# Performance work log

Hardware: AMD Instinct MI355X
Metric: run time of the kernel (lower is better)

The kernel has to match this reference:

```python
import jax, jax.numpy as jnp
import numpy as np

D_EMB = 1024
N_HEADS = 16


def setup_inputs() -> dict:
    key = jax.random.key(0)
    k_x, k_wq, k_bq, k_wp, k_bp = jax.random.split(key, 5)
    B, N, D = 8, 1024, D_EMB
    x = jax.random.normal(k_x, (B, N, D), dtype=jnp.float32)
    s = 1.0 / np.sqrt(D)
    w_qkv = jax.random.normal(k_wq, (D, 3 * D), dtype=jnp.float32) * s
    b_qkv = jax.random.normal(k_bq, (3 * D,), dtype=jnp.float32) * 0.01
    w_proj = jax.random.normal(k_wp, (D, D), dtype=jnp.float32) * s
    b_proj = jax.random.normal(k_bp, (D,), dtype=jnp.float32) * 0.01
    return {"x": x, "w_qkv": w_qkv, "b_qkv": b_qkv, "w_proj": w_proj, "b_proj": b_proj}


def reference(x, w_qkv, b_qkv, w_proj, b_proj):
    B, N, D = x.shape
    H = N_HEADS
    d = D // H
    qkv = x @ w_qkv + b_qkv                      # [B, N, 3D]
    # einops '(h d qkv)': qkv index is the innermost factor of the last dim
    qkv = qkv.reshape(B, N, H, d, 3)
    q = qkv[..., 0]                              # [B, N, H, d]
    k = qkv[..., 1]
    v = qkv[..., 2]
    score = jnp.einsum('bqhd,bkhd->bhqk', q, k)  # [B, H, N, N]
    # module scales AFTER softmax, by sqrt(d_emb) (not sqrt(d_head))
    att = jax.nn.softmax(score, axis=-1) / jnp.sqrt(jnp.float32(D))
    out = jnp.einsum('bhqk,bkhd->bqhd', att, v).reshape(B, N, D)
    return out @ w_proj + b_proj
```

## Files before the change

### kernel.cpp

```cpp
#include <hip/hip_runtime.h>
#include <hip/hip_bf16.h>
#include <stdint.h>

typedef __hip_bfloat16 bf16;
typedef __attribute__((ext_vector_type(8))) short short8;
typedef __attribute__((ext_vector_type(4))) float f32x4;
typedef __attribute__((ext_vector_type(16))) float f32x16;

#define MFMA16(a, b, c) __builtin_amdgcn_mfma_f32_16x16x32_bf16(a, b, c, 0, 0, 0)
#define MFMA32(a, b, c) __builtin_amdgcn_mfma_f32_32x32x16_bf16(a, b, c, 0, 0, 0)

#define BATCH 8
#define SEQ   1024
#define DEMB  1024
#define NH    16
#define DH    64
#define MTOT  (BATCH * SEQ)

__device__ __forceinline__ float rdf(const void* p, size_t idx, int isf) {
  if (isf) return ((const float*)p)[idx];
  return __bfloat162float(((const bf16*)p)[idx]);
}

__device__ __forceinline__ unsigned int pk2(float a, float b) {
  unsigned short ua = __bfloat16_as_ushort(__float2bfloat16(a));
  unsigned short ub = __bfloat16_as_ushort(__float2bfloat16(b));
  return (unsigned int)ua | ((unsigned int)ub << 16);
}

union U4S8 { uint4 u; short8 s; };

__device__ __forceinline__ void gload16(const bf16* g, bf16* l) {
  __builtin_amdgcn_global_load_lds(
      (const __attribute__((address_space(1))) void*)g,
      (__attribute__((address_space(3))) void*)l, 16, 0, 0);
}

__global__ void detect_dtype(const unsigned int* __restrict__ xw, int* __restrict__ flag) {
  int lane = threadIdx.x;
  float v = __uint_as_float(xw[lane]);
  bool isf32 = (fabsf(v) < 1e20f);
  unsigned long long m = __ballot(isf32);
  if (lane == 0) flag[0] = (__popcll(m) >= 32) ? 1 : 0;
}

__global__ __launch_bounds__(256) void convert_x(
    const void* __restrict__ xin, bf16* __restrict__ xc, const int* __restrict__ flag) {
  const int isf = flag[0];
  size_t i = ((size_t)blockIdx.x * 256 + threadIdx.x) * 8;
  if (isf) {
    const float* xf = (const float*)xin;
    float4 a = *(const float4*)&xf[i];
    float4 b = *(const float4*)&xf[i + 4];
    bf16 o[8];
    o[0] = __float2bfloat16(a.x); o[1] = __float2bfloat16(a.y);
    o[2] = __float2bfloat16(a.z); o[3] = __float2bfloat16(a.w);
    o[4] = __float2bfloat16(b.x); o[5] = __float2bfloat16(b.y);
    o[6] = __float2bfloat16(b.z); o[7] = __float2bfloat16(b.w);
    *(int4*)&xc[i] = *(const int4*)&o[0];
  } else {
    *(int4*)&xc[i] = *(const int4*)&((const bf16*)xin)[i];
  }
}

__global__ __launch_bounds__(256) void permute_wqkv(
    const void* __restrict__ w, const void* __restrict__ b,
    bf16* __restrict__ wt, float* __restrict__ bqp, const int* __restrict__ flag) {
  __shared__ __attribute__((aligned(16))) bf16 ls[192][66];
  const int isf = flag[0];
  const int t = threadIdx.x;
  const int k0 = blockIdx.x * 64;
  const int h = blockIdx.y;
#pragma unroll
  for (int i = 0; i < 48; ++i) {
    int e = t + i * 256;
    int k = e / 192, c = e % 192;
    ls[c][k] = __float2bfloat16(rdf(w, (size_t)(k0 + k) * 3072 + h * 192 + c, isf));
  }
  if (blockIdx.x == 0 && t < 192) {
    int dd = t / 3, j = t % 3;
    bqp[j * 1024 + h * 64 + dd] = rdf(b, h * 192 + t, isf);
  }
  __syncthreads();
#pragma unroll
  for (int i = 0; i < 48; ++i) {
    int e = t + i * 256;
    int c = e / 64, k = e & 63;
    int dd = c / 3, j = c % 3;
    wt[(size_t)(j * 1024 + h * 64 + dd) * 1024 + k0 + k] = ls[c][k];
  }
}

__global__ __launch_bounds__(256) void transpose_wp(
    const void* __restrict__ w, bf16* __restrict__ wt, const int* __restrict__ flag) {
  __shared__ __attribute__((aligned(16))) bf16 ls[64][66];
  const int isf = flag[0];
  const int t = threadIdx.x;
  const int r0 = blockIdx.y * 64;
  const int c0 = blockIdx.x * 64;
#pragma unroll
  for (int i = 0; i < 16; ++i) {
    int e = t + i * 256;
    int r = e >> 6, c = e & 63;
    ls[c][r] = __float2bfloat16(rdf(w, (size_t)(r0 + r) * 1024 + c0 + c, isf));
  }
  __syncthreads();
#pragma unroll
  for (int i = 0; i < 16; ++i) {
    int e = t + i * 256;
    int c = e >> 6, r = e & 63;
    wt[(size_t)(c0 + c) * 1024 + r0 + r] = ls[c][r];
  }
}

__device__ __forceinline__ void gemm_core(
    const bf16* __restrict__ A, const bf16* __restrict__ Bt,
    int m0, int n0, f32x4 acc[4][4],
    bf16 lsA[128][32], bf16 lsB[128][32]) {
  const int t = threadIdx.x;
  const int lane = t & 63, w = t >> 6;
  const int quad = lane >> 4, col = lane & 15;
  const int wr = (w >> 1) * 64, wc = (w & 1) * 64;
  const int gr = lane >> 2;
  const int gc = (lane & 3) * 8;
  const bf16* gA = A + (size_t)(m0 + w * 32 + gr) * 1024 + gc;
  const bf16* gB = Bt + (size_t)(n0 + w * 32 + gr) * 1024 + gc;
  bf16* dA0 = &lsA[w * 32][0];
  bf16* dA1 = &lsA[w * 32 + 16][0];
  bf16* dB0 = &lsB[w * 32][0];
  bf16* dB1 = &lsB[w * 32 + 16][0];

  for (int kt = 0; kt < 1024; kt += 32) {
    __syncthreads();
    gload16(gA + kt, dA0);
    gload16(gA + 16 * 1024 + kt, dA1);
    gload16(gB + kt, dB0);
    gload16(gB + 16 * 1024 + kt, dB1);
    __syncthreads();
    short8 af[4], bfr[4];
#pragma unroll
    for (int i = 0; i < 4; ++i) af[i] = *(const short8*)&lsA[wr + i * 16 + col][quad * 8];
#pragma unroll
    for (int j = 0; j < 4; ++j) bfr[j] = *(const short8*)&lsB[wc + j * 16 + col][quad * 8];
#pragma unroll
    for (int i = 0; i < 4; ++i)
#pragma unroll
      for (int j = 0; j < 4; ++j)
        acc[i][j] = MFMA16(af[i], bfr[j], acc[i][j]);
  }
}

__global__ __launch_bounds__(256) void gemm_qkv(
    const bf16* __restrict__ A, const bf16* __restrict__ Bt,
    const float* __restrict__ bias,
    bf16* __restrict__ qb, bf16* __restrict__ kb, bf16* __restrict__ vb) {
  __shared__ __attribute__((aligned(16))) bf16 lsA[128][32];
  __shared__ __attribute__((aligned(16))) bf16 lsB[128][32];
  const int t = threadIdx.x;
  const int lane = t & 63, w = t >> 6;
  const int quad = lane >> 4, col = lane & 15;
  const int wr = (w >> 1) * 64, wc = (w & 1) * 64;
  const int m0 = blockIdx.y * 128;
  const int n0 = blockIdx.x * 128;
  f32x4 acc[4][4];
  const f32x4 zero = {0.f, 0.f, 0.f, 0.f};
#pragma unroll
  for (int i = 0; i < 4; ++i)
#pragma unroll
    for (int j = 0; j < 4; ++j) acc[i][j] = zero;

  gemm_core(A, Bt, m0, n0, acc, lsA, lsB);

  const int jj = n0 >> 10;
#pragma unroll
  for (int i = 0; i < 4; ++i) {
    int rbase = m0 + wr + i * 16 + quad * 4;
#pragma unroll
    for (int j = 0; j < 4; ++j) {
      int c = n0 + wc + j * 16 + col;
      int cc = c & 1023;
      int h = cc >> 6, dd = cc & 63;
      float bv = bias[c];
#pragma unroll
      for (int r = 0; r < 4; ++r) {
        int m = rbase + r;
        int bb = m >> 10, n = m & 1023;
        bf16 val = __float2bfloat16(acc[i][j][r] + bv);
        size_t bhq = (size_t)(bb * NH + h);
        if (jj == 0)      qb[(bhq * 1024 + n) * 64 + dd] = val;
        else if (jj == 1) kb[(bhq * 1024 + n) * 64 + dd] = val;
        else              vb[(bhq * 64 + dd) * 1024 + n] = val;
      }
    }
  }
}

__global__ __launch_bounds__(256, 4) void attn(
    const bf16* __restrict__ qb, const bf16* __restrict__ kb,
    const bf16* __restrict__ vb, bf16* __restrict__ ob) {
  const int t = threadIdx.x, lane = t & 63, w = t >> 6;
  const int q5 = lane & 31, half = lane >> 5;
  const int bh = blockIdx.y;
  const int bat = bh >> 4, h = bh & 15;
  const int q0 = blockIdx.x * 128;
  const int qrow = q0 + w * 32 + q5;

  __shared__ __attribute__((aligned(16))) bf16 lsK[64][72];
  __shared__ __attribute__((aligned(16))) bf16 lsV[64][72];

  const bf16* qp = qb + (size_t)bh * (1024 * 64);
  const bf16* kp = kb + (size_t)bh * (1024 * 64);
  const bf16* vp = vb + (size_t)bh * (64 * 1024);

  short8 bq[4];
#pragma unroll
  for (int kk = 0; kk < 4; ++kk)
    bq[kk] = *(const short8*)&qp[(size_t)qrow * 64 + kk * 16 + half * 8];

  float m_run = -1e30f, l_run = 0.f;
  f32x16 po[2];
#pragma unroll
  for (int r = 0; r < 16; ++r) { po[0][r] = 0.f; po[1][r] = 0.f; }

  const int sr = t >> 3;
  const int sc = (t & 7) * 8;

  for (int kt = 0; kt < 1024; kt += 64) {
    int4 g0 = *(const int4*)&kp[(size_t)(kt + sr) * 64 + sc];
    int4 g1 = *(const int4*)&kp[(size_t)(kt + 32 + sr) * 64 + sc];
    int4 g2 = *(const int4*)&vp[(size_t)sr * 1024 + kt + sc];
    int4 g3 = *(const int4*)&vp[(size_t)(32 + sr) * 1024 + kt + sc];
    __syncthreads();
    *(int4*)&lsK[sr][sc] = g0;
    *(int4*)&lsK[32 + sr][sc] = g1;
    *(int4*)&lsV[sr][sc] = g2;
    *(int4*)&lsV[32 + sr][sc] = g3;
    __syncthreads();

    f32x16 st[2];
#pragma unroll
    for (int r = 0; r < 16; ++r) { st[0][r] = 0.f; st[1][r] = 0.f; }
#pragma unroll
    for (int kk = 0; kk < 4; ++kk) {
#pragma unroll
      for (int tj = 0; tj < 2; ++tj) {
        short8 ak = *(const short8*)&lsK[tj * 32 + q5][kk * 16 + half * 8];
        st[tj] = MFMA32(ak, bq[kk], st[tj]);
      }
    }

    float smax = st[0][0];
#pragma unroll
    for (int r = 1; r < 16; ++r) smax = fmaxf(smax, st[0][r]);
#pragma unroll
    for (int r = 0; r < 16; ++r) smax = fmaxf(smax, st[1][r]);
    smax = fmaxf(smax, __shfl_xor(smax, 32));
    float mnew = fmaxf(m_run, smax);
    float alpha = __expf(m_run - mnew);
    m_run = mnew;
    float lsum = 0.f;
#pragma unroll
    for (int tj = 0; tj < 2; ++tj)
#pragma unroll
      for (int r = 0; r < 16; ++r) {
        float p = __expf(st[tj][r] - mnew);
        st[tj][r] = p;
        lsum += p;
      }
    lsum += __shfl_xor(lsum, 32);
    l_run = l_run * alpha + lsum;
#pragma unroll
    for (int r = 0; r < 16; ++r) { po[0][r] *= alpha; po[1][r] *= alpha; }

#pragma unroll
    for (int kk2 = 0; kk2 < 4; ++kk2) {
      const int nbA = 2 * kk2, nbB = 2 * kk2 + 1;
      unsigned int a0 = pk2(st[nbA >> 2][4 * (nbA & 3) + 0], st[nbA >> 2][4 * (nbA & 3) + 1]);
      unsigned int a1 = pk2(st[nbA >> 2][4 * (nbA & 3) + 2], st[nbA >> 2][4 * (nbA & 3) + 3]);
      unsigned int b0 = pk2(st[nbB >> 2][4 * (nbB & 3) + 0], st[nbB >> 2][4 * (nbB & 3) + 1]);
      unsigned int b1 = pk2(st[nbB >> 2][4 * (nbB & 3) + 2], st[nbB >> 2][4 * (nbB & 3) + 3]);
      unsigned int s0 = half ? a0 : b0;
      unsigned int s1 = half ? a1 : b1;
      unsigned int r0 = (unsigned int)__shfl_xor((int)s0, 32);
      unsigned int r1 = (unsigned int)__shfl_xor((int)s1, 32);
      U4S8 fr;
      fr.u.x = half ? r0 : a0;
      fr.u.y = half ? r1 : a1;
      fr.u.z = half ? b0 : r0;
      fr.u.w = half ? b1 : r1;
#pragma unroll
      for (int ti = 0; ti < 2; ++ti) {
        short8 av = *(const short8*)&lsV[ti * 32 + q5][kk2 * 16 + half * 8];
        po[ti] = MFMA32(av, fr.s, po[ti]);
      }
    }
  }

  float inv = 1.0f / (l_run * 32.0f);
  bf16* op = ob + ((size_t)(bat * 1024 + qrow)) * 1024 + h * 64;
#pragma unroll
  for (int ti = 0; ti < 2; ++ti)
#pragma unroll
    for (int g = 0; g < 4; ++g) {
      unsigned int lo = pk2(po[ti][4 * g + 0] * inv, po[ti][4 * g + 1] * inv);
      unsigned int hi = pk2(po[ti][4 * g + 2] * inv, po[ti][4 * g + 3] * inv);
      uint2 u = make_uint2(lo, hi);
      *(uint2*)&op[ti * 32 + g * 8 + half * 4] = u;
    }
}

__global__ __launch_bounds__(256) void gemm_proj(
    const bf16* __restrict__ A, const bf16* __restrict__ Bt,
    const void* __restrict__ bias, float* __restrict__ out,
    const int* __restrict__ flag) {
  __shared__ __attribute__((aligned(16))) bf16 lsA[128][32];
  __shared__ __attribute__((aligned(16))) bf16 lsB[128][32];
  const int isf = flag[0];
  const int t = threadIdx.x;
  const int lane = t & 63, w = t >> 6;
  const int quad = lane >> 4, col = lane & 15;
  const int wr = (w >> 1) * 64, wc = (w & 1) * 64;
  const int m0 = blockIdx.y * 128;
  const int n0 = blockIdx.x * 128;
  f32x4 acc[4][4];
  const f32x4 zero = {0.f, 0.f, 0.f, 0.f};
#pragma unroll
  for (int i = 0; i < 4; ++i)
#pragma unroll
    for (int j = 0; j < 4; ++j) acc[i][j] = zero;

  gemm_core(A, Bt, m0, n0, acc, lsA, lsB);

#pragma unroll
  for (int i = 0; i < 4; ++i) {
    int rbase = m0 + wr + i * 16 + quad * 4;
#pragma unroll
    for (int j = 0; j < 4; ++j) {
      int c = n0 + wc + j * 16 + col;
      float bv = rdf(bias, c, isf);
#pragma unroll
      for (int r = 0; r < 4; ++r)
        out[(size_t)(rbase + r) * 1024 + c] = acc[i][j][r] + bv;
    }
  }
}

extern "C" void kernel_launch(void* const* d_in, const int* in_sizes, int n_in,
                              void* d_out, int out_size, void* d_ws, size_t ws_size,
                              hipStream_t stream) {
  const void* x      = d_in[0];
  const void* w_qkv  = d_in[1];
  const void* b_qkv  = d_in[2];
  const void* w_proj = d_in[3];
  const void* b_proj = d_in[4];
  float* out = (float*)d_out;

  char* ws = (char*)d_ws;
  bf16*  wt_qkv = (bf16*)(ws);
  float* bqp    = (float*)(ws + 6291456);
  bf16*  wtp    = (bf16*)(ws + 6303744);
  bf16*  xc     = (bf16*)(ws + 8400896);
  bf16*  q_buf  = (bf16*)(ws + 25178112);
  bf16*  k_buf  = (bf16*)(ws + 41955328);
  bf16*  v_buf  = (bf16*)(ws + 58732544);
  int*   flag   = (int*)(ws + 75509760);
  bf16*  att    = xc;

  detect_dtype<<<1, 64, 0, stream>>>((const unsigned int*)x, flag);
  convert_x<<<4096, 256, 0, stream>>>(x, xc, flag);
  permute_wqkv<<<dim3(16, 16), 256, 0, stream>>>(w_qkv, b_qkv, wt_qkv, bqp, flag);
  transpose_wp<<<dim3(16, 16), 256, 0, stream>>>(w_proj, wtp, flag);
  gemm_qkv<<<dim3(24, 64), 256, 0, stream>>>(xc, wt_qkv, bqp, q_buf, k_buf, v_buf);
  attn<<<dim3(8, 128), 256, 0, stream>>>(q_buf, k_buf, v_buf, att);
  gemm_proj<<<dim3(8, 64), 256, 0, stream>>>(att, wtp, b_proj, out, flag);
}
```

Baseline: 301.4 us.

## Replace GEMM core with 256x256 tiles and a 4-stage LDS pipeline

```diff
diff --git a/kernel.cpp b/kernel.cpp
--- a/kernel.cpp
+++ b/kernel.cpp
@@ -113,83 +113,126 @@
   }
 }
 
-__device__ __forceinline__ void gemm_core(
+__device__ __forceinline__ void gemm256_core(
     const bf16* __restrict__ A, const bf16* __restrict__ Bt,
-    int m0, int n0, f32x4 acc[4][4],
-    bf16 lsA[128][32], bf16 lsB[128][32]) {
+    int m0, int n0, bf16* lds, f32x4 acc[8][4]) {
   const int t = threadIdx.x;
   const int lane = t & 63, w = t >> 6;
-  const int quad = lane >> 4, col = lane & 15;
-  const int wr = (w >> 1) * 64, wc = (w & 1) * 64;
-  const int gr = lane >> 2;
-  const int gc = (lane & 3) * 8;
-  const bf16* gA = A + (size_t)(m0 + w * 32 + gr) * 1024 + gc;
-  const bf16* gB = Bt + (size_t)(n0 + w * 32 + gr) * 1024 + gc;
-  bf16* dA0 = &lsA[w * 32][0];
-  bf16* dA1 = &lsA[w * 32 + 16][0];
-  bf16* dB0 = &lsB[w * 32][0];
-  bf16* dB1 = &lsB[w * 32 + 16][0];
-
-  for (int kt = 0; kt < 1024; kt += 32) {
-    __syncthreads();
-    gload16(gA + kt, dA0);
-    gload16(gA + 16 * 1024 + kt, dA1);
-    gload16(gB + kt, dB0);
-    gload16(gB + 16 * 1024 + kt, dB1);
-    __syncthreads();
-    short8 af[4], bfr[4];
-#pragma unroll
-    for (int i = 0; i < 4; ++i) af[i] = *(const short8*)&lsA[wr + i * 16 + col][quad * 8];
-#pragma unroll
-    for (int j = 0; j < 4; ++j) bfr[j] = *(const short8*)&lsB[wc + j * 16 + col][quad * 8];
+  const int l15 = lane & 15, quad = lane >> 4;
+  const int wm = w >> 2, wn = w & 3;
+
+  const int sr = lane >> 2;
+  const int sc = (lane & 3) * 8;
+  const bf16* gA = A + (size_t)(m0 + w * 16 + sr) * 1024 + sc;
+  const bf16* gB = Bt + (size_t)(n0 + w * 16 + sr) * 1024 + sc;
+
+#pragma unroll
+  for (int tt = 0; tt < 3; ++tt) {
+    bf16* sb = lds + tt * 16384;
+    gload16(gA + tt * 32, sb + w * 512);
+    gload16(gA + tt * 32 + 131072, sb + 4096 + w * 512);
+    gload16(gB + tt * 32, sb + 8192 + w * 512);
+    gload16(gB + tt * 32 + 131072, sb + 12288 + w * 512);
+  }
+  asm volatile("s_waitcnt vmcnt(8)" ::: "memory");
+  __builtin_amdgcn_s_barrier();
+
+#pragma unroll 4
+  for (int tau = 0; tau < 32; ++tau) {
+    const int slot = tau & 3;
+    const int pf = (tau + 3) & 3;
+    const int kpf = ((tau + 3) & 31) * 32;
+    const bf16* ls = lds + slot * 16384;
+    bf16* sb = lds + pf * 16384;
+
+    short8 afr[4], bfr[4];
+    const bf16* pa0 = ls + (wm * 128 + l15) * 32 + quad * 8;
+#pragma unroll
+    for (int i = 0; i < 4; ++i) afr[i] = *(const short8*)(pa0 + i * 512);
+    const bf16* pb0 = ls + 8192 + (wn * 64 + l15) * 32 + quad * 8;
+#pragma unroll
+    for (int j = 0; j < 4; ++j) bfr[j] = *(const short8*)(pb0 + j * 512);
+    gload16(gA + kpf, sb + w * 512);
+    gload16(gA + kpf + 131072, sb + 4096 + w * 512);
+    asm volatile("" ::: "memory");
+    __builtin_amdgcn_s_barrier();
+    asm volatile("s_waitcnt lgkmcnt(0)" ::: "memory");
+    __builtin_amdgcn_s_setprio(1);
 #pragma unroll
     for (int i = 0; i < 4; ++i)
 #pragma unroll
       for (int j = 0; j < 4; ++j)
-        acc[i][j] = MFMA16(af[i], bfr[j], acc[i][j]);
-  }
-}
-
-__global__ __launch_bounds__(256) void gemm_qkv(
+        acc[i][j] = MFMA16(afr[i], bfr[j], acc[i][j]);
+    __builtin_amdgcn_s_setprio(0);
+    asm volatile("" ::: "memory");
+    __builtin_amdgcn_s_barrier();
+
+    const bf16* pa1 = pa0 + 64 * 32;
+#pragma unroll
+    for (int i = 0; i < 4; ++i) afr[i] = *(const short8*)(pa1 + i * 512);
+    gload16(gB + kpf, sb + 8192 + w * 512);
+    gload16(gB + kpf + 131072, sb + 12288 + w * 512);
+    asm volatile("" ::: "memory");
+    __builtin_amdgcn_s_barrier();
+    asm volatile("s_waitcnt lgkmcnt(0)" ::: "memory");
+    __builtin_amdgcn_s_setprio(1);
+#pragma unroll
+    for (int i = 0; i < 4; ++i)
+#pragma unroll
+      for (int j = 0; j < 4; ++j)
+        acc[4 + i][j] = MFMA16(afr[i], bfr[j], acc[4 + i][j]);
+    __builtin_amdgcn_s_setprio(0);
+    asm volatile("s_waitcnt vmcnt(8)" ::: "memory");
+    asm volatile("" ::: "memory");
+    __builtin_amdgcn_s_barrier();
+  }
+  asm volatile("s_waitcnt vmcnt(0)" ::: "memory");
+}
+
+__global__ __launch_bounds__(512, 2) void gemm256_qkv(
     const bf16* __restrict__ A, const bf16* __restrict__ Bt,
     const float* __restrict__ bias,
     bf16* __restrict__ qb, bf16* __restrict__ kb, bf16* __restrict__ vb) {
-  __shared__ __attribute__((aligned(16))) bf16 lsA[128][32];
-  __shared__ __attribute__((aligned(16))) bf16 lsB[128][32];
+  extern __shared__ bf16 smem[];
   const int t = threadIdx.x;
-  const int lane = t & 63, w = t >> 6;
-  const int quad = lane >> 4, col = lane & 15;
-  const int wr = (w >> 1) * 64, wc = (w & 1) * 64;
-  const int m0 = blockIdx.y * 128;
-  const int n0 = blockIdx.x * 128;
-  f32x4 acc[4][4];
+  const int lane = t & 63;
+  const int l15 = lane & 15, quad = lane >> 4;
+  const int w = t >> 6, wm = w >> 2, wn = w & 3;
+  const int bid = blockIdx.x;
+  const int swz = (bid & 7) * 48 + (bid >> 3);
+  const int m0 = (swz / 12) * 256;
+  const int n0 = (swz % 12) * 256;
+
+  f32x4 acc[8][4];
   const f32x4 zero = {0.f, 0.f, 0.f, 0.f};
 #pragma unroll
-  for (int i = 0; i < 4; ++i)
+  for (int i = 0; i < 8; ++i)
 #pragma unroll
     for (int j = 0; j < 4; ++j) acc[i][j] = zero;
 
-  gemm_core(A, Bt, m0, n0, acc, lsA, lsB);
+  gemm256_core(A, Bt, m0, n0, smem, acc);
 
   const int jj = n0 >> 10;
-#pragma unroll
-  for (int i = 0; i < 4; ++i) {
-    int rbase = m0 + wr + i * 16 + quad * 4;
-#pragma unroll
-    for (int j = 0; j < 4; ++j) {
-      int c = n0 + wc + j * 16 + col;
-      int cc = c & 1023;
-      int h = cc >> 6, dd = cc & 63;
-      float bv = bias[c];
-#pragma unroll
-      for (int r = 0; r < 4; ++r) {
-        int m = rbase + r;
-        int bb = m >> 10, n = m & 1023;
-        bf16 val = __float2bfloat16(acc[i][j][r] + bv);
-        size_t bhq = (size_t)(bb * NH + h);
-        if (jj == 0)      qb[(bhq * 1024 + n) * 64 + dd] = val;
-        else if (jj == 1) kb[(bhq * 1024 + n) * 64 + dd] = val;
-        else              vb[(bhq * 64 + dd) * 1024 + n] = val;
+  const int hh = ((n0 + wn * 64) & 1023) >> 6;
+#pragma unroll
+  for (int fi = 0; fi < 8; ++fi) {
+    int m = m0 + wm * 128 + fi * 16 + quad * 4;
+    int bb = m >> 10, nidx = m & 1023;
+    size_t bhq = (size_t)(bb * NH + hh);
+#pragma unroll
+    for (int fj = 0; fj < 4; ++fj) {
+      int dd = fj * 16 + l15;
+      float bv = bias[n0 + wn * 64 + dd];
+      if (jj == 2) {
+        unsigned int lo = pk2(acc[fi][fj][0] + bv, acc[fi][fj][1] + bv);
+        unsigned int hi = pk2(acc[fi][fj][2] + bv, acc[fi][fj][3] + bv);
+        *(uint2*)&vb[(bhq * 64 + dd) * 1024 + nidx] = make_uint2(lo, hi);
+      } else {
+        bf16* dst = (jj == 0) ? qb : kb;
+#pragma unroll
+        for (int r = 0; r < 4; ++r)
+          dst[(bhq * 1024 + (size_t)(nidx + r)) * 64 + dd] =
+              __float2bfloat16(acc[fi][fj][r] + bv);
       }
     }
   }
@@ -309,38 +352,40 @@
     }
 }
 
-__global__ __launch_bounds__(256) void gemm_proj(
+__global__ __launch_bounds__(512, 2) void gemm256_proj(
     const bf16* __restrict__ A, const bf16* __restrict__ Bt,
     const void* __restrict__ bias, float* __restrict__ out,
     const int* __restrict__ flag) {
-  __shared__ __attribute__((aligned(16))) bf16 lsA[128][32];
-  __shared__ __attribute__((aligned(16))) bf16 lsB[128][32];
+  extern __shared__ bf16 smem[];
+  const int t = threadIdx.x;
+  const int lane = t & 63;
+  const int l15 = lane & 15, quad = lane >> 4;
+  const int w = t >> 6, wm = w >> 2, wn = w & 3;
+  const int bid = blockIdx.x;
+  const int swz = (bid & 7) * 16 + (bid >> 3);
+  const int m0 = (swz >> 2) * 256;
+  const int n0 = (swz & 3) * 256;
+
+  f32x4 acc[8][4];
+  const f32x4 zero = {0.f, 0.f, 0.f, 0.f};
+#pragma unroll
+  for (int i = 0; i < 8; ++i)
+#pragma unroll
+    for (int j = 0; j < 4; ++j) acc[i][j] = zero;
+
+  gemm256_core(A, Bt, m0, n0, smem, acc);
+
   const int isf = flag[0];
-  const int t = threadIdx.x;
-  const int lane = t & 63, w = t >> 6;
-  const int quad = lane >> 4, col = lane & 15;
-  const int wr = (w >> 1) * 64, wc = (w & 1) * 64;
-  const int m0 = blockIdx.y * 128;
-  const int n0 = blockIdx.x * 128;
-  f32x4 acc[4][4];
-  const f32x4 zero = {0.f, 0.f, 0.f, 0.f};
-#pragma unroll
-  for (int i = 0; i < 4; ++i)
-#pragma unroll
-    for (int j = 0; j < 4; ++j) acc[i][j] = zero;
-
-  gemm_core(A, Bt, m0, n0, acc, lsA, lsB);
-
-#pragma unroll
-  for (int i = 0; i < 4; ++i) {
-    int rbase = m0 + wr + i * 16 + quad * 4;
-#pragma unroll
-    for (int j = 0; j < 4; ++j) {
-      int c = n0 + wc + j * 16 + col;
-      float bv = rdf(bias, c, isf);
+#pragma unroll
+  for (int fj = 0; fj < 4; ++fj) {
+    int c = n0 + wn * 64 + fj * 16 + l15;
+    float bv = rdf(bias, c, isf);
+#pragma unroll
+    for (int fi = 0; fi < 8; ++fi) {
+      int m = m0 + wm * 128 + fi * 16 + quad * 4;
 #pragma unroll
       for (int r = 0; r < 4; ++r)
-        out[(size_t)(rbase + r) * 1024 + c] = acc[i][j][r] + bv;
+        out[(size_t)(m + r) * 1024 + c] = acc[fi][fj][r] + bv;
     }
   }
 }
@@ -366,11 +411,20 @@
   int*   flag   = (int*)(ws + 75509760);
   bf16*  att    = xc;
 
+  static bool lds_attr_done = false;
+  if (!lds_attr_done) {
+    (void)hipFuncSetAttribute(reinterpret_cast<const void*>(gemm256_qkv),
+                              hipFuncAttributeMaxDynamicSharedMemorySize, 131072);
+    (void)hipFuncSetAttribute(reinterpret_cast<const void*>(gemm256_proj),
+                              hipFuncAttributeMaxDynamicSharedMemorySize, 131072);
+    lds_attr_done = true;
+  }
+
   detect_dtype<<<1, 64, 0, stream>>>((const unsigned int*)x, flag);
   convert_x<<<4096, 256, 0, stream>>>(x, xc, flag);
   permute_wqkv<<<dim3(16, 16), 256, 0, stream>>>(w_qkv, b_qkv, wt_qkv, bqp, flag);
   transpose_wp<<<dim3(16, 16), 256, 0, stream>>>(w_proj, wtp, flag);
-  gemm_qkv<<<dim3(24, 64), 256, 0, stream>>>(xc, wt_qkv, bqp, q_buf, k_buf, v_buf);
+  gemm256_qkv<<<dim3(384), 512, 131072, stream>>>(xc, wt_qkv, bqp, q_buf, k_buf, v_buf);
   attn<<<dim3(8, 128), 256, 0, stream>>>(q_buf, k_buf, v_buf, att);
-  gemm_proj<<<dim3(8, 64), 256, 0, stream>>>(att, wtp, b_proj, out, flag);
-}
+  gemm256_proj<<<dim3(128), 512, 131072, stream>>>(att, wtp, b_proj, out, flag);
+}
```

Measured after the change: 289.0 us. -4.1%, faster.
